# Performance work log

Measured on AMD Instinct MI355X. Metric: run time of the kernel, lower is better.

## Reference

```python
import jax, jax.numpy as jnp
import numpy as np

B, T, H, L_DIM, O = 256, 512, 256, 128, 1


def setup_inputs() -> dict:
    key = jax.random.key(0)
    ks = jax.random.split(key, 12)
    s_h = 1.0 / np.sqrt(H)
    s_l = np.sqrt(6.0 / (L_DIM + H))   # xavier_uniform for latent_to_hidden
    s_o = np.sqrt(6.0 / (H + O))       # xavier_uniform for hidden_to_output
    return {
        "latent": jax.random.normal(ks[0], (B, L_DIM), dtype=jnp.float32),
        "W_lh": jax.random.uniform(ks[1], (H, L_DIM), jnp.float32, -s_l, s_l),
        "b_lh": jnp.zeros((H,), jnp.float32),
        # LSTM layer 0 (input_size=1, but inputs are all-zero)
        "W_ih0": jax.random.uniform(ks[2], (4 * H, 1), jnp.float32, -s_h, s_h),
        "W_hh0": jax.random.uniform(ks[3], (4 * H, H), jnp.float32, -s_h, s_h),
        "b_ih0": jax.random.uniform(ks[4], (4 * H,), jnp.float32, -s_h, s_h),
        "b_hh0": jax.random.uniform(ks[5], (4 * H,), jnp.float32, -s_h, s_h),
        # LSTM layer 1 (input_size=H)
        "W_ih1": jax.random.uniform(ks[6], (4 * H, H), jnp.float32, -s_h, s_h),
        "W_hh1": jax.random.uniform(ks[7], (4 * H, H), jnp.float32, -s_h, s_h),
        "b_ih1": jax.random.uniform(ks[8], (4 * H,), jnp.float32, -s_h, s_h),
        "b_hh1": jax.random.uniform(ks[9], (4 * H,), jnp.float32, -s_h, s_h),
        "W_ho": jax.random.uniform(ks[10], (O, H), jnp.float32, -s_o, s_o),
        "b_ho": jnp.zeros((O,), jnp.float32),
    }


def _cell(x_contrib, h, c, W_hh, b):
    # torch gate order: i, f, g, o
    z = x_contrib + h @ W_hh.T + b  # [B, 4H]
    i, f, g, o = jnp.split(z, 4, axis=-1)
    c = jax.nn.sigmoid(f) * c + jax.nn.sigmoid(i) * jnp.tanh(g)
    h = jax.nn.sigmoid(o) * jnp.tanh(c)
    return h, c


def reference(latent, W_lh, b_lh, W_ih0, W_hh0, b_ih0, b_hh0,
              W_ih1, W_hh1, b_ih1, b_hh1, W_ho, b_ho):
    # h_0 for every layer = latent_to_hidden(latent); c_0 = 0
    h_init = latent @ W_lh.T + b_lh  # [B, H]
    c0 = jnp.zeros_like(h_init)
    b0 = b_ih0 + b_hh0  # layer-0 input is all-zero, so W_ih0 @ x == 0
    b1 = b_ih1 + b_hh1

    def step(carry, _):
        h0, c0_, h1, c1 = carry
        h0, c0_ = _cell(b0[None, :], h0, c0_, W_hh0, jnp.zeros((4 * H,), h0.dtype))
        h1, c1 = _cell(h0 @ W_ih1.T, h1, c1, W_hh1, b1)
        return (h0, c0_, h1, c1), h1

    _, hs = jax.lax.scan(step, (h_init, c0, h_init, c0), None, length=T)
    hs = jnp.transpose(hs, (1, 0, 2))  # [B, T, H]
    return hs @ W_ho.T + b_ho          # [B, T, O]
```

## Files before the change

kernel.cpp:

```cpp
#include <hip/hip_runtime.h>
#include <cstdint>

#define TT 512

typedef unsigned short u16;
typedef uint32_t u32;
typedef float    floatx4 __attribute__((ext_vector_type(4)));
typedef _Float16 f16x8   __attribute__((ext_vector_type(8)));
typedef short    short8  __attribute__((ext_vector_type(8)));
typedef u32      u32x4   __attribute__((ext_vector_type(4)));
typedef u32      u32x2   __attribute__((ext_vector_type(2)));

__device__ __forceinline__ float sigm(float x)  { return 1.0f / (1.0f + __expf(-x)); }
__device__ __forceinline__ float tanh_(float x) { return 2.0f / (1.0f + __expf(-2.0f * x)) - 1.0f; }
__device__ __forceinline__ u16 f2h(float f) {
    union { _Float16 h; u16 u; } v; v.h = (_Float16)f; return v.u;
}
#define F16V(p) (*(const f16x8*)(const void*)(p))

__device__ __forceinline__ void st32_dev(u32* p, u32 v) {
    asm volatile("global_store_dword %0, %1, off sc1" :: "v"(p), "v"(v) : "memory");
}
__device__ __forceinline__ void st64_dev(u32* p, u32 lo, u32 hi) {
    u32x2 d; d[0] = lo; d[1] = hi;
    asm volatile("global_store_dwordx2 %0, %1, off sc1" :: "v"(p), "v"(d) : "memory");
}
__device__ __forceinline__ u32x4 ld128_dev(const u32x4* p) {
    u32x4 v;
    asm volatile("global_load_dwordx4 %0, %1, off sc1" : "=v"(v) : "v"(p));
    return v;
}
__device__ __forceinline__ u32 ld32_dev(const u32* p) {
    u32 v;
    asm volatile("global_load_dword %0, %1, off sc1" : "=v"(v) : "v"(p));
    return v;
}
__device__ __forceinline__ void vmcnt0() { asm volatile("s_waitcnt vmcnt(0)" ::: "memory"); }
#define KEEP(x) asm volatile("" : "+v"(x))

__global__ void zero_ws(u32* base, int n4) {
    u32x4 z = {0u, 0u, 0u, 0u};
    for (int i = blockIdx.x * blockDim.x + threadIdx.x; i < n4; i += gridDim.x * blockDim.x)
        asm volatile("global_store_dwordx4 %0, %1, off sc1"
                     :: "v"(((u32x4*)base) + i), "v"(z) : "memory");
}

#define MFMA_(A_, B_, ACC) ACC = __builtin_amdgcn_mfma_f32_16x16x32_f16(A_, B_, ACC, 0, 0, 0)
#define MS1(ACC, GATE_) { f16x8 A_ = F16V(fs0 + (GATE_) * 4096); MFMA_(A_, Bh, ACC); }
#define MS3(ACC, GATE_) { f16x8 A1_ = F16V(fs1 + (GATE_) * 4096); MFMA_(A1_, Bh, ACC); \
    f16x8 A2_ = F16V(fs2 + (GATE_) * 4096); MFMA_(A2_, Ch, ACC); }

#define GATE0(R) { \
    const int d_ = dg16 + 4 * q + (R); \
    float zi_ = Zi[R] + bs[0][d_], zf_ = Zf[R] + bs[1][d_]; \
    float zg_ = Zg[R] + bs[2][d_], zo_ = Zo[R] + bs[3][d_]; \
    float c_  = sigm(zf_) * cv[R] + sigm(zi_) * tanh_(zg_); cv[R] = c_; \
    float hv_ = sigm(zo_) * tanh_(c_); \
    st32_dev(&hx0w[d_ * 16 + bq], tgthi | (u32)f2h(hv_)); }
#define GATE1(R) { \
    const int d_ = dg16 + 4 * q + (R); \
    float zi_ = Yi[R] + bs[0][d_], zf_ = Yf[R] + bs[1][d_]; \
    float zg_ = Yg[R] + bs[2][d_], zo_ = Yo[R] + bs[3][d_]; \
    float c_  = sigm(zf_) * cv[R] + sigm(zi_) * tanh_(zg_); cv[R] = c_; \
    float hv_ = sigm(zo_) * tanh_(c_); \
    st32_dev(&hx1w[d_ * 16 + bq], tgthi | (u32)f2h(hv_)); \
    part += hv_ * who_s[d_]; }

#define UNPACK0(v, i4) { const int d_ = (i4) >> 2, bb_ = ((i4) & 3) * 4; \
    h0f[bb_ + 0][d_] = (u16)((v)[0] & 0xFFFFu); \
    h0f[bb_ + 1][d_] = (u16)((v)[1] & 0xFFFFu); \
    h0f[bb_ + 2][d_] = (u16)((v)[2] & 0xFFFFu); \
    h0f[bb_ + 3][d_] = (u16)((v)[3] & 0xFFFFu); }
#define UNPACK1(v, i4) { const int d_ = (i4) >> 2, bb_ = ((i4) & 3) * 4; \
    h1f[bb_ + 0][d_] = (u16)((v)[0] & 0xFFFFu); \
    h1f[bb_ + 1][d_] = (u16)((v)[1] & 0xFFFFu); \
    h1f[bb_ + 2][d_] = (u16)((v)[2] & 0xFFFFu); \
    h1f[bb_ + 3][d_] = (u16)((v)[3] & 0xFFFFu); }
#define STALE4(v) (((v)[0] ^ tgthi) | ((v)[1] ^ tgthi) | ((v)[2] ^ tgthi) | ((v)[3] ^ tgthi))

__launch_bounds__(128, 1)
__global__ void lstm_wave(const float* __restrict__ latent, const float* __restrict__ W_lh,
                          const float* __restrict__ b_lh,
                          const float* __restrict__ W_hh0,
                          const float* __restrict__ b_ih0, const float* __restrict__ b_hh0,
                          const float* __restrict__ W_ih1, const float* __restrict__ W_hh1,
                          const float* __restrict__ b_ih1, const float* __restrict__ b_hh1,
                          const float* __restrict__ W_ho,  const float* __restrict__ b_ho,
                          u32* __restrict__ hx0, u32* __restrict__ hx1,
                          u32* __restrict__ posc, float* __restrict__ out)
{
    extern __shared__ __align__(16) char smem[];
    short* wlds     = (short*)smem;
    u16 (*h0f)[264] = (u16(*)[264])(smem + 131072);
    u16 (*h1f)[264] = (u16(*)[264])(smem + 139520);
    float (*bs)[256] = (float(*)[256])(smem + 147968);
    float* who_s    = (float*)(smem + 152064);

    const int tid  = threadIdx.x;
    const int w    = tid >> 6;
    const int lane = tid & 63;
    const int bq   = lane & 15;
    const int q    = lane >> 4;
    const int g    = blockIdx.x & 15;
    const int s16  = blockIdx.x >> 4;
    const int role = s16 >> 3;
    const int jl   = s16 & 7;
    const int bglo = g * 16;

    {
        const int nv = role ? 8192 : 4096;
        for (int i = tid; i < nv; i += 128) {
            const int l8 = i & 63, s8 = (i >> 6) & 7, gate8 = (i >> 9) & 3;
            const int dgl = (i >> 11) & 1, G = (i >> 12) & 1;
            const float* W = role ? (G ? W_hh1 : W_ih1) : W_hh0;
            const int rowdim = jl * 32 + dgl * 16 + (l8 & 15);
            const float* src = W + (gate8 * 256 + rowdim) * 256 + s8 * 32 + (l8 >> 4) * 8;
            short8 v;
#pragma unroll
            for (int jj = 0; jj < 8; ++jj) v[jj] = (short)f2h(src[jj]);
            *(short8*)(wlds + l8 * 8 + s8 * 512 + gate8 * 4096 + dgl * 16384 + G * 32768) = v;
        }
    }
    for (int i = tid; i < 1024; i += 128)
        bs[i >> 8][i & 255] = role ? (b_ih1[i] + b_hh1[i]) : (b_ih0[i] + b_hh0[i]);
    if (role) { who_s[tid] = W_ho[tid]; who_s[tid + 128] = W_ho[tid + 128]; }

    {
        const int b = tid >> 3, d0 = (tid & 7) * 32;
        const float* lr = latent + (bglo + b) * 128;
        for (int jj = 0; jj < 32; ++jj) {
            const int d = d0 + jj;
            const float* wr = W_lh + d * 128;
            float acc = b_lh[d];
            for (int c = 0; c < 128; c += 4) {
                float4 lv = *(const float4*)(lr + c);
                float4 wv = *(const float4*)(wr + c);
                acc += lv.x * wv.x + lv.y * wv.y + lv.z * wv.z + lv.w * wv.w;
            }
            u16 hb = f2h(acc);
            h0f[b][d] = hb;
            if (role) h1f[b][d] = hb;
        }
    }
    __syncthreads();

    const int dg16 = jl * 32 + w * 16;
    const short* fbA = wlds + w * 16384 + (size_t)lane * 8;
    float cv[4] = {0.f, 0.f, 0.f, 0.f};
    const float bho = b_ho[0];

    if (role == 0) {
        for (int p = 0; p < TT; ++p) {
            const int pb = p & 1;
            u32* hx0w = hx0 + pb * 65536 + g * 4096;
            const u32* hx1w = hx1 + pb * 65536 + g * 4096;
            const u32 tgthi = (u32)(p + 1) << 16;
            const u32 tgt32 = (u32)(p + 1);

            floatx4 Zi = {0.f,0.f,0.f,0.f}, Zf = {0.f,0.f,0.f,0.f};
            floatx4 Zg = {0.f,0.f,0.f,0.f}, Zo = {0.f,0.f,0.f,0.f};
#pragma unroll
            for (int s = 0; s < 8; ++s) {
                f16x8 Bh = F16V(&h0f[bq][s * 32 + q * 8]);
                const short* fs0 = fbA + s * 512;
                MS1(Zi, 0) MS1(Zf, 1) MS1(Zg, 2) MS1(Zo, 3)
            }
            GATE0(0) GATE0(1) GATE0(2) GATE0(3)
            if (p == TT - 1) break;

            u32x4 va0, va1, va2, va3, va4, va5, va6, va7;
            u32 pc = 0;
            const u32x4* s4a = (const u32x4*)hx0w;
#define ISSUE0() do { \
            va0 = ld128_dev(s4a + tid);       va1 = ld128_dev(s4a + tid + 128); \
            va2 = ld128_dev(s4a + tid + 256); va3 = ld128_dev(s4a + tid + 384); \
            va4 = ld128_dev(s4a + tid + 512); va5 = ld128_dev(s4a + tid + 640); \
            va6 = ld128_dev(s4a + tid + 768); va7 = ld128_dev(s4a + tid + 896); \
            if ((lane < 8) && p) pc = ld32_dev(hx1w + lane * 512); \
        } while (0)
            ISSUE0();
            __syncthreads();
            int it = 0;
            while (true) {
                vmcnt0();
                KEEP(va0); KEEP(va1); KEEP(va2); KEEP(va3);
                KEEP(va4); KEEP(va5); KEEP(va6); KEEP(va7); KEEP(pc);
                u32 sh = STALE4(va0) | STALE4(va1) | STALE4(va2) | STALE4(va3)
                       | STALE4(va4) | STALE4(va5) | STALE4(va6) | STALE4(va7);
                const bool okp = ((lane < 8) && p) ? ((pc >> 16) >= tgt32) : true;
                const bool ok = ((sh & 0xFFFF0000u) == 0u) && okp;
                if (__ballot(ok) == 0xFFFFFFFFFFFFFFFFull) break;
                if (++it > 20000) break;
                ISSUE0();
            }
#undef ISSUE0
            UNPACK0(va0, tid);       UNPACK0(va1, tid + 128);
            UNPACK0(va2, tid + 256); UNPACK0(va3, tid + 384);
            UNPACK0(va4, tid + 512); UNPACK0(va5, tid + 640);
            UNPACK0(va6, tid + 768); UNPACK0(va7, tid + 896);
            __syncthreads();
        }
    } else {
        const short* fbB = fbA;
        const bool isout = (jl == 0);
        for (int p = 0; p <= TT; ++p) {
            const int pb = p & 1;
            const u32* hx0w = hx0 + pb * 65536 + g * 4096;
            u32* hx1w = hx1 + pb * 65536 + g * 4096;
            u32* poscw = posc + (pb * 16 + g) * 512;
            const u32 tgthi = (u32)(p + 1) << 16;
            const u32 tgt32 = (u32)(p + 1);

            if (p >= 1) {
                floatx4 Yi = {0.f,0.f,0.f,0.f}, Yf = {0.f,0.f,0.f,0.f};
                floatx4 Yg = {0.f,0.f,0.f,0.f}, Yo = {0.f,0.f,0.f,0.f};
#pragma unroll
                for (int s = 0; s < 8; ++s) {
                    f16x8 Bh = F16V(&h0f[bq][s * 32 + q * 8]);
                    f16x8 Ch = F16V(&h1f[bq][s * 32 + q * 8]);
                    const short* fs1 = fbB + s * 512;
                    const short* fs2 = fs1 + 32768;
                    MS3(Yi, 0) MS3(Yf, 1) MS3(Yg, 2) MS3(Yo, 3)
                }
                float part = 0.0f;
                GATE1(0) GATE1(1) GATE1(2) GATE1(3)
                part += __shfl_xor(part, 16, 64);
                part += __shfl_xor(part, 32, 64);
                if (q == 0)
                    st64_dev(poscw + (bq * 16 + jl * 2 + w) * 2,
                             __float_as_uint(part), tgt32);
            }

            const bool rdA = p < TT;
            const bool rdB = (p >= 1) && (p < TT);
            const bool rdP = isout && (p >= 1) && (tid < 16);
            u32x4 va0, va1, va2, va3, va4, va5, va6, va7;
            u32x4 vb0, vb1, vb2, vb3, vb4, vb5, vb6, vb7;
            u32x4 po0, po1, po2, po3, po4, po5, po6, po7;
            const u32x4* s4a = (const u32x4*)hx0w;
            const u32x4* s4b = (const u32x4*)hx1w;
            const u32x4* s4p = (const u32x4*)poscw + tid * 8;
#define ISSUE1() do { \
            if (rdA) { \
                va0 = ld128_dev(s4a + tid);       va1 = ld128_dev(s4a + tid + 128); \
                va2 = ld128_dev(s4a + tid + 256); va3 = ld128_dev(s4a + tid + 384); \
                va4 = ld128_dev(s4a + tid + 512); va5 = ld128_dev(s4a + tid + 640); \
                va6 = ld128_dev(s4a + tid + 768); va7 = ld128_dev(s4a + tid + 896); } \
            if (rdB) { \
                vb0 = ld128_dev(s4b + tid);       vb1 = ld128_dev(s4b + tid + 128); \
                vb2 = ld128_dev(s4b + tid + 256); vb3 = ld128_dev(s4b + tid + 384); \
                vb4 = ld128_dev(s4b + tid + 512); vb5 = ld128_dev(s4b + tid + 640); \
                vb6 = ld128_dev(s4b + tid + 768); vb7 = ld128_dev(s4b + tid + 896); } \
            if (rdP) { \
                po0 = ld128_dev(s4p);     po1 = ld128_dev(s4p + 1); \
                po2 = ld128_dev(s4p + 2); po3 = ld128_dev(s4p + 3); \
                po4 = ld128_dev(s4p + 4); po5 = ld128_dev(s4p + 5); \
                po6 = ld128_dev(s4p + 6); po7 = ld128_dev(s4p + 7); } \
        } while (0)
            ISSUE1();
            __syncthreads();
            int it = 0;
            while (true) {
                vmcnt0();
                u32 sh = 0, sf = 0;
                if (rdA) {
                    KEEP(va0); KEEP(va1); KEEP(va2); KEEP(va3);
                    KEEP(va4); KEEP(va5); KEEP(va6); KEEP(va7);
                    sh |= STALE4(va0) | STALE4(va1) | STALE4(va2) | STALE4(va3)
                        | STALE4(va4) | STALE4(va5) | STALE4(va6) | STALE4(va7);
                }
                if (rdB) {
                    KEEP(vb0); KEEP(vb1); KEEP(vb2); KEEP(vb3);
                    KEEP(vb4); KEEP(vb5); KEEP(vb6); KEEP(vb7);
                    sh |= STALE4(vb0) | STALE4(vb1) | STALE4(vb2) | STALE4(vb3)
                        | STALE4(vb4) | STALE4(vb5) | STALE4(vb6) | STALE4(vb7);
                }
                if (rdP) {
                    KEEP(po0); KEEP(po1); KEEP(po2); KEEP(po3);
                    KEEP(po4); KEEP(po5); KEEP(po6); KEEP(po7);
                    sf |= (po0[1] ^ tgt32) | (po0[3] ^ tgt32) | (po1[1] ^ tgt32) | (po1[3] ^ tgt32)
                        | (po2[1] ^ tgt32) | (po2[3] ^ tgt32) | (po3[1] ^ tgt32) | (po3[3] ^ tgt32)
                        | (po4[1] ^ tgt32) | (po4[3] ^ tgt32) | (po5[1] ^ tgt32) | (po5[3] ^ tgt32)
                        | (po6[1] ^ tgt32) | (po6[3] ^ tgt32) | (po7[1] ^ tgt32) | (po7[3] ^ tgt32);
                }
                const bool ok = ((sh & 0xFFFF0000u) == 0u) && (sf == 0u);
                if (__ballot(ok) == 0xFFFFFFFFFFFFFFFFull) break;
                if (++it > 20000) break;
                ISSUE1();
            }
#undef ISSUE1
            if (rdA) {
                UNPACK0(va0, tid);       UNPACK0(va1, tid + 128);
                UNPACK0(va2, tid + 256); UNPACK0(va3, tid + 384);
                UNPACK0(va4, tid + 512); UNPACK0(va5, tid + 640);
                UNPACK0(va6, tid + 768); UNPACK0(va7, tid + 896);
            }
            if (rdB) {
                UNPACK1(vb0, tid);       UNPACK1(vb1, tid + 128);
                UNPACK1(vb2, tid + 256); UNPACK1(vb3, tid + 384);
                UNPACK1(vb4, tid + 512); UNPACK1(vb5, tid + 640);
                UNPACK1(vb6, tid + 768); UNPACK1(vb7, tid + 896);
            }
            if (rdP) {
                float o = bho;
                o += __uint_as_float(po0[0]) + __uint_as_float(po0[2]);
                o += __uint_as_float(po1[0]) + __uint_as_float(po1[2]);
                o += __uint_as_float(po2[0]) + __uint_as_float(po2[2]);
                o += __uint_as_float(po3[0]) + __uint_as_float(po3[2]);
                o += __uint_as_float(po4[0]) + __uint_as_float(po4[2]);
                o += __uint_as_float(po5[0]) + __uint_as_float(po5[2]);
                o += __uint_as_float(po6[0]) + __uint_as_float(po6[2]);
                o += __uint_as_float(po7[0]) + __uint_as_float(po7[2]);
                out[(bglo + tid) * TT + (p - 1)] = o;
            }
            __syncthreads();
        }
    }
}

extern "C" void kernel_launch(void* const* d_in, const int* in_sizes, int n_in,
                              void* d_out, int out_size, void* d_ws, size_t ws_size,
                              hipStream_t stream)
{
    const float* latent = (const float*)d_in[0];
    const float* W_lh   = (const float*)d_in[1];
    const float* b_lh   = (const float*)d_in[2];
    const float* W_hh0  = (const float*)d_in[4];
    const float* b_ih0  = (const float*)d_in[5];
    const float* b_hh0  = (const float*)d_in[6];
    const float* W_ih1  = (const float*)d_in[7];
    const float* W_hh1  = (const float*)d_in[8];
    const float* b_ih1  = (const float*)d_in[9];
    const float* b_hh1  = (const float*)d_in[10];
    const float* W_ho   = (const float*)d_in[11];
    const float* b_ho   = (const float*)d_in[12];

    char* ws = (char*)d_ws;
    u32*   hx0  = (u32*)ws;
    u32*   hx1  = (u32*)(ws + 524288);
    u32*   posc = (u32*)(ws + 1048576);

    hipFuncSetAttribute((const void*)lstm_wave,
                        hipFuncAttributeMaxDynamicSharedMemorySize, 153088);

    zero_ws<<<dim3(128), dim3(256), 0, stream>>>(hx0, 69632);
    lstm_wave<<<dim3(256), dim3(128), 153088, stream>>>(latent, W_lh, b_lh,
                                                        W_hh0, b_ih0, b_hh0,
                                                        W_ih1, W_hh1, b_ih1, b_hh1,
                                                        W_ho, b_ho,
                                                        hx0, hx1, posc,
                                                        (float*)d_out);
}
```

Baseline: 2.086 ms.

## Quad-buffer inter-block exchange, loosen layer-0 pacing, poll only stale buffers

Increases the hx0/hx1/posc exchange buffers from double to quadruple buffering so the layer-0 producer may run up to two steps ahead of layer 1 rather than waiting on it every step. The spin-wait loops now track readiness per buffer (A, B, output partials) and reissue loads only for buffers still stale, which cuts redundant global polling traffic. The cost is doubled workspace and a larger zeroing kernel, and correctness depends on the ring depth being enough for the looser lag bound.

New measurement: 8.178 ms. +292.0%, slower.

```diff
diff --git a/kernel.cpp b/kernel.cpp
--- a/kernel.cpp
+++ b/kernel.cpp
@@ -148,12 +148,12 @@
     const short* fbA = wlds + w * 16384 + (size_t)lane * 8;
     float cv[4] = {0.f, 0.f, 0.f, 0.f};
     const float bho = b_ho[0];
+    const unsigned long long ALL = 0xFFFFFFFFFFFFFFFFull;
 
     if (role == 0) {
         for (int p = 0; p < TT; ++p) {
-            const int pb = p & 1;
+            const int pb = p & 3;
             u32* hx0w = hx0 + pb * 65536 + g * 4096;
-            const u32* hx1w = hx1 + pb * 65536 + g * 4096;
             const u32 tgthi = (u32)(p + 1) << 16;
             const u32 tgt32 = (u32)(p + 1);
 
@@ -171,29 +171,39 @@
             u32x4 va0, va1, va2, va3, va4, va5, va6, va7;
             u32 pc = 0;
             const u32x4* s4a = (const u32x4*)hx0w;
-#define ISSUE0() do { \
+            const u32* pacep = hx1 + ((p - 2) & 3) * 65536 + g * 4096 + lane * 512;
+            const bool dopace = (lane < 8) && (p >= 2);
+#define ISSA() do { \
             va0 = ld128_dev(s4a + tid);       va1 = ld128_dev(s4a + tid + 128); \
             va2 = ld128_dev(s4a + tid + 256); va3 = ld128_dev(s4a + tid + 384); \
             va4 = ld128_dev(s4a + tid + 512); va5 = ld128_dev(s4a + tid + 640); \
             va6 = ld128_dev(s4a + tid + 768); va7 = ld128_dev(s4a + tid + 896); \
-            if ((lane < 8) && p) pc = ld32_dev(hx1w + lane * 512); \
         } while (0)
-            ISSUE0();
+            ISSA();
+            if (dopace) pc = ld32_dev(pacep);
             __syncthreads();
+            bool dA = false, dP = false;
             int it = 0;
             while (true) {
                 vmcnt0();
-                KEEP(va0); KEEP(va1); KEEP(va2); KEEP(va3);
-                KEEP(va4); KEEP(va5); KEEP(va6); KEEP(va7); KEEP(pc);
-                u32 sh = STALE4(va0) | STALE4(va1) | STALE4(va2) | STALE4(va3)
-                       | STALE4(va4) | STALE4(va5) | STALE4(va6) | STALE4(va7);
-                const bool okp = ((lane < 8) && p) ? ((pc >> 16) >= tgt32) : true;
-                const bool ok = ((sh & 0xFFFF0000u) == 0u) && okp;
-                if (__ballot(ok) == 0xFFFFFFFFFFFFFFFFull) break;
+                if (!dA) {
+                    KEEP(va0); KEEP(va1); KEEP(va2); KEEP(va3);
+                    KEEP(va4); KEEP(va5); KEEP(va6); KEEP(va7);
+                    u32 sh = STALE4(va0) | STALE4(va1) | STALE4(va2) | STALE4(va3)
+                           | STALE4(va4) | STALE4(va5) | STALE4(va6) | STALE4(va7);
+                    if (__ballot((sh & 0xFFFF0000u) == 0u) == ALL) dA = true;
+                }
+                if (!dP) {
+                    KEEP(pc);
+                    const bool okp = dopace ? ((pc >> 16) + 2u >= tgt32) : true;
+                    if (__ballot(okp) == ALL) dP = true;
+                }
+                if (dA && dP) break;
                 if (++it > 20000) break;
-                ISSUE0();
-            }
-#undef ISSUE0
+                if (!dA) ISSA();
+                if (!dP && dopace) pc = ld32_dev(pacep);
+            }
+#undef ISSA
             UNPACK0(va0, tid);       UNPACK0(va1, tid + 128);
             UNPACK0(va2, tid + 256); UNPACK0(va3, tid + 384);
             UNPACK0(va4, tid + 512); UNPACK0(va5, tid + 640);
@@ -204,7 +214,7 @@
         const short* fbB = fbA;
         const bool isout = (jl == 0);
         for (int p = 0; p <= TT; ++p) {
-            const int pb = p & 1;
+            const int pb = p & 3;
             const u32* hx0w = hx0 + pb * 65536 + g * 4096;
             u32* hx1w = hx1 + pb * 65536 + g * 4096;
             u32* poscw = posc + (pb * 16 + g) * 512;
@@ -240,55 +250,67 @@
             const u32x4* s4a = (const u32x4*)hx0w;
             const u32x4* s4b = (const u32x4*)hx1w;
             const u32x4* s4p = (const u32x4*)poscw + tid * 8;
-#define ISSUE1() do { \
-            if (rdA) { \
-                va0 = ld128_dev(s4a + tid);       va1 = ld128_dev(s4a + tid + 128); \
-                va2 = ld128_dev(s4a + tid + 256); va3 = ld128_dev(s4a + tid + 384); \
-                va4 = ld128_dev(s4a + tid + 512); va5 = ld128_dev(s4a + tid + 640); \
-                va6 = ld128_dev(s4a + tid + 768); va7 = ld128_dev(s4a + tid + 896); } \
-            if (rdB) { \
-                vb0 = ld128_dev(s4b + tid);       vb1 = ld128_dev(s4b + tid + 128); \
-                vb2 = ld128_dev(s4b + tid + 256); vb3 = ld128_dev(s4b + tid + 384); \
-                vb4 = ld128_dev(s4b + tid + 512); vb5 = ld128_dev(s4b + tid + 640); \
-                vb6 = ld128_dev(s4b + tid + 768); vb7 = ld128_dev(s4b + tid + 896); } \
-            if (rdP) { \
-                po0 = ld128_dev(s4p);     po1 = ld128_dev(s4p + 1); \
-                po2 = ld128_dev(s4p + 2); po3 = ld128_dev(s4p + 3); \
-                po4 = ld128_dev(s4p + 4); po5 = ld128_dev(s4p + 5); \
-                po6 = ld128_dev(s4p + 6); po7 = ld128_dev(s4p + 7); } \
+#define ISSA() do { \
+            va0 = ld128_dev(s4a + tid);       va1 = ld128_dev(s4a + tid + 128); \
+            va2 = ld128_dev(s4a + tid + 256); va3 = ld128_dev(s4a + tid + 384); \
+            va4 = ld128_dev(s4a + tid + 512); va5 = ld128_dev(s4a + tid + 640); \
+            va6 = ld128_dev(s4a + tid + 768); va7 = ld128_dev(s4a + tid + 896); \
         } while (0)
-            ISSUE1();
+#define ISSB() do { \
+            vb0 = ld128_dev(s4b + tid);       vb1 = ld128_dev(s4b + tid + 128); \
+            vb2 = ld128_dev(s4b + tid + 256); vb3 = ld128_dev(s4b + tid + 384); \
+            vb4 = ld128_dev(s4b + tid + 512); vb5 = ld128_dev(s4b + tid + 640); \
+            vb6 = ld128_dev(s4b + tid + 768); vb7 = ld128_dev(s4b + tid + 896); \
+        } while (0)
+#define ISSP() do { \
+            po0 = ld128_dev(s4p);     po1 = ld128_dev(s4p + 1); \
+            po2 = ld128_dev(s4p + 2); po3 = ld128_dev(s4p + 3); \
+            po4 = ld128_dev(s4p + 4); po5 = ld128_dev(s4p + 5); \
+            po6 = ld128_dev(s4p + 6); po7 = ld128_dev(s4p + 7); \
+        } while (0)
+            if (rdA) ISSA();
+            if (rdB) ISSB();
+            if (rdP) ISSP();
             __syncthreads();
+            bool dA = !rdA, dB = !rdB, dP = !(isout && (p >= 1));
             int it = 0;
             while (true) {
                 vmcnt0();
-                u32 sh = 0, sf = 0;
-                if (rdA) {
+                if (!dA) {
                     KEEP(va0); KEEP(va1); KEEP(va2); KEEP(va3);
                     KEEP(va4); KEEP(va5); KEEP(va6); KEEP(va7);
-                    sh |= STALE4(va0) | STALE4(va1) | STALE4(va2) | STALE4(va3)
-                        | STALE4(va4) | STALE4(va5) | STALE4(va6) | STALE4(va7);
-                }
-                if (rdB) {
+                    u32 sh = STALE4(va0) | STALE4(va1) | STALE4(va2) | STALE4(va3)
+                           | STALE4(va4) | STALE4(va5) | STALE4(va6) | STALE4(va7);
+                    if (__ballot((sh & 0xFFFF0000u) == 0u) == ALL) dA = true;
+                }
+                if (!dB) {
                     KEEP(vb0); KEEP(vb1); KEEP(vb2); KEEP(vb3);
                     KEEP(vb4); KEEP(vb5); KEEP(vb6); KEEP(vb7);
-                    sh |= STALE4(vb0) | STALE4(vb1) | STALE4(vb2) | STALE4(vb3)
-                        | STALE4(vb4) | STALE4(vb5) | STALE4(vb6) | STALE4(vb7);
-                }
-                if (rdP) {
-                    KEEP(po0); KEEP(po1); KEEP(po2); KEEP(po3);
-                    KEEP(po4); KEEP(po5); KEEP(po6); KEEP(po7);
-                    sf |= (po0[1] ^ tgt32) | (po0[3] ^ tgt32) | (po1[1] ^ tgt32) | (po1[3] ^ tgt32)
-                        | (po2[1] ^ tgt32) | (po2[3] ^ tgt32) | (po3[1] ^ tgt32) | (po3[3] ^ tgt32)
-                        | (po4[1] ^ tgt32) | (po4[3] ^ tgt32) | (po5[1] ^ tgt32) | (po5[3] ^ tgt32)
-                        | (po6[1] ^ tgt32) | (po6[3] ^ tgt32) | (po7[1] ^ tgt32) | (po7[3] ^ tgt32);
-                }
-                const bool ok = ((sh & 0xFFFF0000u) == 0u) && (sf == 0u);
-                if (__ballot(ok) == 0xFFFFFFFFFFFFFFFFull) break;
+                    u32 sh = STALE4(vb0) | STALE4(vb1) | STALE4(vb2) | STALE4(vb3)
+                           | STALE4(vb4) | STALE4(vb5) | STALE4(vb6) | STALE4(vb7);
+                    if (__ballot((sh & 0xFFFF0000u) == 0u) == ALL) dB = true;
+                }
+                if (!dP) {
+                    u32 sf = 0;
+                    if (rdP) {
+                        KEEP(po0); KEEP(po1); KEEP(po2); KEEP(po3);
+                        KEEP(po4); KEEP(po5); KEEP(po6); KEEP(po7);
+                        sf = (po0[1] ^ tgt32) | (po0[3] ^ tgt32) | (po1[1] ^ tgt32) | (po1[3] ^ tgt32)
+                           | (po2[1] ^ tgt32) | (po2[3] ^ tgt32) | (po3[1] ^ tgt32) | (po3[3] ^ tgt32)
+                           | (po4[1] ^ tgt32) | (po4[3] ^ tgt32) | (po5[1] ^ tgt32) | (po5[3] ^ tgt32)
+                           | (po6[1] ^ tgt32) | (po6[3] ^ tgt32) | (po7[1] ^ tgt32) | (po7[3] ^ tgt32);
+                    }
+                    if (__ballot(sf == 0u) == ALL) dP = true;
+                }
+                if (dA && dB && dP) break;
                 if (++it > 20000) break;
-                ISSUE1();
-            }
-#undef ISSUE1
+                if (!dA) ISSA();
+                if (!dB) ISSB();
+                if (!dP && rdP) ISSP();
+            }
+#undef ISSA
+#undef ISSB
+#undef ISSP
             if (rdA) {
                 UNPACK0(va0, tid);       UNPACK0(va1, tid + 128);
                 UNPACK0(va2, tid + 256); UNPACK0(va3, tid + 384);
@@ -337,13 +359,13 @@
 
     char* ws = (char*)d_ws;
     u32*   hx0  = (u32*)ws;
-    u32*   hx1  = (u32*)(ws + 524288);
-    u32*   posc = (u32*)(ws + 1048576);
+    u32*   hx1  = (u32*)(ws + 1048576);
+    u32*   posc = (u32*)(ws + 2097152);
 
     hipFuncSetAttribute((const void*)lstm_wave,
                         hipFuncAttributeMaxDynamicSharedMemorySize, 153088);
 
-    zero_ws<<<dim3(128), dim3(256), 0, stream>>>(hx0, 69632);
+    zero_ws<<<dim3(128), dim3(256), 0, stream>>>(hx0, 139264);
     lstm_wave<<<dim3(256), dim3(128), 153088, stream>>>(latent, W_lh, b_lh,
                                                         W_hh0, b_ih0, b_hh0,
                                                         W_ih1, W_hh1, b_ih1, b_hh1,
```
